# Kernel optimization log

Measured on AMD Instinct MI355X. Metric: run time of the kernel, lower is better.

## Reference

```python
import jax, jax.numpy as jnp
import numpy as np
import itertools

B, G, FEAT, IMG = 2048, 8, 512, 1024
SCALES = list(range(G, 1, -1))  # [8,7,6,5,4,3,2]
SUBSAMPLE = 12


def setup_inputs() -> dict:
    key = jax.random.key(0)
    keys = jax.random.split(key, 1 + 2 * len(SCALES))
    rng = np.random.default_rng(0)
    inp = {"input": jax.random.normal(keys[0], (B, G, FEAT), dtype=jnp.float32)}
    for i, scale in enumerate(SCALES):
        perms = np.array(list(itertools.permutations(range(G), scale)), dtype=np.int32)
        n_sub = min(SUBSAMPLE, len(perms))
        sel = rng.choice(len(perms), n_sub, replace=False)
        inp[f"perms{i}"] = jnp.asarray(perms[sel])  # [n_sub, scale] int32
        lim = 1.0 / np.sqrt(scale * FEAT)
        inp[f"W{i}"] = jax.random.uniform(keys[1 + 2 * i], (IMG, scale * FEAT), minval=-lim, maxval=lim, dtype=jnp.float32)
        inp[f"b{i}"] = jax.random.uniform(keys[2 + 2 * i], (IMG,), minval=-lim, maxval=lim, dtype=jnp.float32)
    return inp


def _forward(input, perms_list, W_list, b_list):
    outs = []
    for perms, W, b in zip(perms_list, W_list, b_list):
        # gather: [B, n_sub, scale, FEAT] -> [B, n_sub, scale*FEAT]
        g = input[:, perms, :]
        g = g.reshape(g.shape[0], g.shape[1], -1)
        # batched linear over all subsamples, then mean over subsamples
        y = jnp.einsum('bsf,df->bsd', g, W) + b  # [B, n_sub, IMG]
        outs.append(y.mean(axis=1))
    return jnp.concatenate(outs, axis=1)  # [B, len(SCALES)*IMG]


def reference(input, perms0, W0, b0, perms1, W1, b1, perms2, W2, b2,
              perms3, W3, b3, perms4, W4, b4, perms5, W5, b5, perms6, W6, b6):
    perms_list = [perms0, perms1, perms2, perms3, perms4, perms5, perms6]
    W_list = [W0, W1, W2, W3, W4, W5, W6]
    b_list = [b0, b1, b2, b3, b4, b5, b6]
    return _forward(input, perms_list, W_list, b_list)
```

## Files before the change

### kernel.cpp

```cpp
#include <hip/hip_runtime.h>

typedef unsigned short u16;
typedef __bf16 bf16x8 __attribute__((ext_vector_type(8)));
typedef float f32x4 __attribute__((ext_vector_type(4)));

__device__ __forceinline__ u16 f2bf(float f) {
  unsigned int u = __float_as_uint(f);
  return (u16)((u + 0x7fffu + ((u >> 16) & 1u)) >> 16);
}


__global__ __launch_bounds__(256) void k_prep(
    const float* __restrict__ x,
    const int* p0, const int* p1, const int* p2, const int* p3,
    const int* p4, const int* p5, const int* p6,
    const float* W0, const float* W1, const float* W2, const float* W3,
    const float* W4, const float* W5, const float* W6,
    u16* __restrict__ Xb16, u16* __restrict__ Wtil) {
  __shared__ float sC[64];
  const int bid = blockIdx.x;
  const int t = threadIdx.x;
  if (bid < 1792) {
    const int r0 = bid << 2;
    const int i = r0 >> 10;
    const int scale = 8 - i;
    const int K = scale << 9;
    const int d0 = r0 - (i << 10);
    if (t < 64) {
      const int g = t >> 3, j = t & 7;
      float v = 0.f;
      if (j < scale) {
        const int* p = (i == 0) ? p0 : (i == 1) ? p1 : (i == 2) ? p2 :
                       (i == 3) ? p3 : (i == 4) ? p4 : (i == 5) ? p5 : p6;
        int cnt = 0;
        for (int s = 0; s < 12; ++s) cnt += (p[s * scale + j] == g) ? 1 : 0;
        v = (float)cnt * (1.0f / 12.0f);
      }
      sC[t] = v;
    }
    __syncthreads();
    const float* Wi = (i == 0) ? W0 : (i == 1) ? W1 : (i == 2) ? W2 :
                      (i == 3) ? W3 : (i == 4) ? W4 : (i == 5) ? W5 : W6;
    const int u = t & 63;
    const int gq = t >> 6;
    u16* dst = Wtil + ((size_t)r0 << 12);
    for (int r = 0; r < 4; ++r) {
      const float* wrow = Wi + (size_t)(d0 + r) * K;
      float a0[8], a1[8];
#pragma unroll
      for (int e = 0; e < 8; ++e) { a0[e] = 0.f; a1[e] = 0.f; }
      for (int j = 0; j < scale; ++j) {
        const float* wp = wrow + j * 512 + (u << 3);
        const float4 wa = *reinterpret_cast<const float4*>(wp);
        const float4 wb = *reinterpret_cast<const float4*>(wp + 4);
        const float c0 = sC[(gq << 4) + j];
        const float c1 = sC[(gq << 4) + 8 + j];
        a0[0] += c0 * wa.x; a0[1] += c0 * wa.y; a0[2] += c0 * wa.z; a0[3] += c0 * wa.w;
        a0[4] += c0 * wb.x; a0[5] += c0 * wb.y; a0[6] += c0 * wb.z; a0[7] += c0 * wb.w;
        a1[0] += c1 * wa.x; a1[1] += c1 * wa.y; a1[2] += c1 * wa.z; a1[3] += c1 * wa.w;
        a1[4] += c1 * wb.x; a1[5] += c1 * wb.y; a1[6] += c1 * wb.z; a1[7] += c1 * wb.w;
      }
      uint4 o0, o1;
      o0.x = (unsigned)f2bf(a0[0]) | ((unsigned)f2bf(a0[1]) << 16);
      o0.y = (unsigned)f2bf(a0[2]) | ((unsigned)f2bf(a0[3]) << 16);
      o0.z = (unsigned)f2bf(a0[4]) | ((unsigned)f2bf(a0[5]) << 16);
      o0.w = (unsigned)f2bf(a0[6]) | ((unsigned)f2bf(a0[7]) << 16);
      o1.x = (unsigned)f2bf(a1[0]) | ((unsigned)f2bf(a1[1]) << 16);
      o1.y = (unsigned)f2bf(a1[2]) | ((unsigned)f2bf(a1[3]) << 16);
      o1.z = (unsigned)f2bf(a1[4]) | ((unsigned)f2bf(a1[5]) << 16);
      o1.w = (unsigned)f2bf(a1[6]) | ((unsigned)f2bf(a1[7]) << 16);
      u16* drow = dst + ((size_t)r << 12) + (gq << 10) + (u << 3);
      *reinterpret_cast<uint4*>(drow) = o0;
      *reinterpret_cast<uint4*>(drow + 512) = o1;
    }
  } else {
    const int tid0 = ((bid - 1792) << 8) | t;
    const float4* X4 = reinterpret_cast<const float4*>(x);
    uint4* O = reinterpret_cast<uint4*>(Xb16);
#pragma unroll 4
    for (int it = 0; it < 16; ++it) {
      const int e = tid0 + (it << 16);
      const float4 a = X4[(size_t)e * 2];
      const float4 c = X4[(size_t)e * 2 + 1];
      uint4 o;
      o.x = (unsigned)f2bf(a.x) | ((unsigned)f2bf(a.y) << 16);
      o.y = (unsigned)f2bf(a.z) | ((unsigned)f2bf(a.w) << 16);
      o.z = (unsigned)f2bf(c.x) | ((unsigned)f2bf(c.y) << 16);
      o.w = (unsigned)f2bf(c.z) | ((unsigned)f2bf(c.w) << 16);
      O[e] = o;
    }
  }
}

__device__ __forceinline__ void gl_lds16(const u16* g, u16* l) {
  __builtin_amdgcn_global_load_lds(
      (const __attribute__((address_space(1))) void*)g,
      (__attribute__((address_space(3))) void*)l, 16, 0, 0);
}

#define WAIT_VM10  0x0F7A
#define WAIT_VM8   0x0F78
#define WAIT_VM4   0x0F74
#define WAIT_VM2   0x0F72
#define WAIT_VM0   0x0F70
#define WAIT_LGKM0 0xC07F

#define MFMA_Q(QD, AV, BV)                                                   \
  _Pragma("unroll")                                                          \
  for (int mf_ = 0; mf_ < 4; ++mf_) {                                        \
    _Pragma("unroll")                                                        \
    for (int nf_ = 0; nf_ < 2; ++nf_) {                                      \
      acc[QD][mf_][nf_] = __builtin_amdgcn_mfma_f32_16x16x32_bf16(           \
          AV[mf_][0], BV[nf_][0], acc[QD][mf_][nf_], 0, 0, 0);               \
      acc[QD][mf_][nf_] = __builtin_amdgcn_mfma_f32_16x16x32_bf16(           \
          AV[mf_][1], BV[nf_][1], acc[QD][mf_][nf_], 0, 0, 0);               \
    }                                                                        \
  }

#define RD_A(BASE)                                                           \
  _Pragma("unroll")                                                          \
  for (int mf_ = 0; mf_ < 4; ++mf_) {                                        \
    aR[mf_][0] = *reinterpret_cast<const bf16x8*>(lds + (BASE) + offA[mf_]);        \
    aR[mf_][1] = *reinterpret_cast<const bf16x8*>(lds + (BASE) + (offA[mf_] ^ 32)); \
  }

#define RD_B(BASE, ARR)                                                      \
  _Pragma("unroll")                                                          \
  for (int nf_ = 0; nf_ < 2; ++nf_) {                                        \
    ARR[nf_][0] = *reinterpret_cast<const bf16x8*>(lds + (BASE) + offB[nf_]);        \
    ARR[nf_][1] = *reinterpret_cast<const bf16x8*>(lds + (BASE) + (offB[nf_] ^ 32)); \
  }

#define PH_BAR  __builtin_amdgcn_s_barrier()
#define PH_LGKM __builtin_amdgcn_s_waitcnt(WAIT_LGKM0)
#define PRIO1   __builtin_amdgcn_s_setprio(1)
#define PRIO0   __builtin_amdgcn_s_setprio(0)

__global__ __launch_bounds__(512, 2) void k_gemm(
    const u16* __restrict__ A, const u16* __restrict__ Bm,
    const float* b0, const float* b1, const float* b2, const float* b3,
    const float* b4, const float* b5, const float* b6,
    float* __restrict__ out) {
  __shared__ u16 lds[65536];
  const int bid = blockIdx.x;
  const int blockM = (bid & 7) * 256;
  const int blockN = (bid >> 3) * 256;

  const int tid = threadIdx.x;
  const int lane = tid & 63;
  const int wid = tid >> 6;
  const int wm = (wid >> 2) * 64;
  const int wn = (wid & 3) * 32;
  const int quad = lane >> 4;
  const int l15 = lane & 15;

  const int srow = tid >> 3;
  const int sslot = tid & 7;
  const int gch = (sslot - srow) & 7;
  const u16* gA0 = A + (size_t)(blockM + srow) * 4096 + gch * 8;
  const u16* gB0 = Bm + (size_t)(blockN + srow) * 4096 + gch * 8;

  int offA[4], offB[2];
#pragma unroll
  for (int mf = 0; mf < 4; ++mf) {
    const int r = wm + mf * 16 + l15;
    offA[mf] = r * 64 + ((quad + r) & 7) * 8;
  }
#pragma unroll
  for (int nf = 0; nf < 2; ++nf) {
    const int r = wn + nf * 16 + l15;
    offB[nf] = 16384 + r * 64 + ((quad + r) & 7) * 8;
  }

  f32x4 acc[4][4][2];
#pragma unroll
  for (int q = 0; q < 4; ++q)
#pragma unroll
    for (int m = 0; m < 4; ++m)
#pragma unroll
      for (int n = 0; n < 2; ++n) {
        f32x4 z = {0.f, 0.f, 0.f, 0.f};
        acc[q][m][n] = z;
      }

  auto stage = [&](int mat, int h, int t, int db) {
    const u16* g = (mat ? gB0 : gA0) + (size_t)h * (128 * 4096) + (size_t)t * 64;
    u16* l = lds + db + mat * 16384 + h * 8192 + (tid << 3);
    gl_lds16(g, l);
    gl_lds16(g + (size_t)(64 * 4096), l + 4096);
  };

  stage(0, 0, 0, 0); stage(1, 0, 0, 0); stage(1, 1, 0, 0); stage(0, 1, 0, 0);
  stage(0, 0, 1, 32768); stage(1, 0, 1, 32768); stage(1, 1, 1, 32768);
  __builtin_amdgcn_s_waitcnt(WAIT_VM10);
  PH_BAR;

  bf16x8 aR[4][2], bL[2][2], bH[2][2];

  for (int j = 0; j < 31; ++j) {
    const int t1 = 2 * j + 1;
    const int t2 = 2 * j + 2;
    const int t3 = 2 * j + 3;

    RD_A(0) RD_B(0, bL)
    stage(0, 1, t1, 32768);
    PH_BAR; PH_LGKM; PRIO1; MFMA_Q(0, aR, bL) PRIO0;
    __builtin_amdgcn_s_waitcnt(WAIT_VM10); PH_BAR;

    RD_B(8192, bH)
    stage(0, 0, t2, 0);
    PH_BAR; PH_LGKM; PRIO1; MFMA_Q(1, aR, bH) PRIO0;
    __builtin_amdgcn_s_waitcnt(WAIT_VM10); PH_BAR;

    RD_A(8192)
    stage(1, 0, t2, 0);
    PH_BAR; PH_LGKM; PRIO1; MFMA_Q(2, aR, bH) PRIO0;
    PH_BAR;

    stage(1, 1, t2, 0);
    PH_BAR; PRIO1; MFMA_Q(3, aR, bL) PRIO0;
    __builtin_amdgcn_s_waitcnt(WAIT_VM10); PH_BAR;

    RD_A(32768) RD_B(32768, bL)
    stage(0, 1, t2, 0);
    PH_BAR; PH_LGKM; PRIO1; MFMA_Q(0, aR, bL) PRIO0;
    __builtin_amdgcn_s_waitcnt(WAIT_VM10); PH_BAR;

    RD_B(32768 + 8192, bH)
    stage(0, 0, t3, 32768);
    PH_BAR; PH_LGKM; PRIO1; MFMA_Q(1, aR, bH) PRIO0;
    __builtin_amdgcn_s_waitcnt(WAIT_VM10); PH_BAR;

    RD_A(32768 + 8192)
    stage(1, 0, t3, 32768);
    PH_BAR; PH_LGKM; PRIO1; MFMA_Q(2, aR, bH) PRIO0;
    PH_BAR;

    stage(1, 1, t3, 32768);
    PH_BAR; PRIO1; MFMA_Q(3, aR, bL) PRIO0;
    __builtin_amdgcn_s_waitcnt(WAIT_VM10); PH_BAR;
  }

  {
    RD_A(0) RD_B(0, bL)
    stage(0, 1, 63, 32768);
    PH_BAR; PH_LGKM; PRIO1; MFMA_Q(0, aR, bL) PRIO0;
    __builtin_amdgcn_s_waitcnt(WAIT_VM10); PH_BAR;

    RD_B(8192, bH)
    PH_BAR; PH_LGKM; PRIO1; MFMA_Q(1, aR, bH) PRIO0;
    __builtin_amdgcn_s_waitcnt(WAIT_VM8); PH_BAR;

    RD_A(8192)
    PH_BAR; PH_LGKM; PRIO1; MFMA_Q(2, aR, bH) PRIO0;
    PH_BAR;

    PH_BAR; PRIO1; MFMA_Q(3, aR, bL) PRIO0;
    __builtin_amdgcn_s_waitcnt(WAIT_VM4); PH_BAR;

    RD_A(32768) RD_B(32768, bL)
    PH_BAR; PH_LGKM; PRIO1; MFMA_Q(0, aR, bL) PRIO0;
    __builtin_amdgcn_s_waitcnt(WAIT_VM2); PH_BAR;

    RD_B(32768 + 8192, bH)
    PH_BAR; PH_LGKM; PRIO1; MFMA_Q(1, aR, bH) PRIO0;
    __builtin_amdgcn_s_waitcnt(WAIT_VM0); PH_BAR;

    RD_A(32768 + 8192)
    PH_BAR; PH_LGKM; PRIO1; MFMA_Q(2, aR, bH) PRIO0;
    PH_BAR;

    PRIO1; MFMA_Q(3, aR, bL) PRIO0;
  }

  const int isc = blockN >> 10;
  const float* bi = (isc == 0) ? b0 : (isc == 1) ? b1 : (isc == 2) ? b2 :
                    (isc == 3) ? b3 : (isc == 4) ? b4 : (isc == 5) ? b5 : b6;
#pragma unroll
  for (int qd = 0; qd < 4; ++qd) {
    const int Mq = (qd >= 2) ? 128 : 0;
    const int Nq = (qd == 1 || qd == 2) ? 128 : 0;
#pragma unroll
    for (int nf = 0; nf < 2; ++nf) {
      const int ncol = blockN + Nq + wn + nf * 16 + l15;
      const float bias = bi[ncol & 1023];
#pragma unroll
      for (int mf = 0; mf < 4; ++mf) {
        const int mbase = blockM + Mq + wm + mf * 16 + quad * 4;
#pragma unroll
        for (int reg = 0; reg < 4; ++reg)
          out[(size_t)(mbase + reg) * 7168 + ncol] = acc[qd][mf][nf][reg] + bias;
      }
    }
  }
}

extern "C" void kernel_launch(void* const* d_in, const int* in_sizes, int n_in,
                              void* d_out, int out_size, void* d_ws, size_t ws_size,
                              hipStream_t stream) {
  const float* input = (const float*)d_in[0];
  const int* perms[7];
  const float* W[7];
  const float* bias[7];
  for (int i = 0; i < 7; ++i) {
    perms[i] = (const int*)d_in[1 + 3 * i];
    W[i]     = (const float*)d_in[2 + 3 * i];
    bias[i]  = (const float*)d_in[3 + 3 * i];
  }
  char* ws = (char*)d_ws;
  u16* Xb16 = (u16*)ws;
  u16* Wtil = (u16*)(ws + (size_t)2048 * 4096 * 2);

  k_prep<<<2048, 256, 0, stream>>>(input,
                                   perms[0], perms[1], perms[2], perms[3],
                                   perms[4], perms[5], perms[6],
                                   W[0], W[1], W[2], W[3], W[4], W[5], W[6],
                                   Xb16, Wtil);
  k_gemm<<<224, 512, 0, stream>>>(Xb16, Wtil,
                                  bias[0], bias[1], bias[2], bias[3],
                                  bias[4], bias[5], bias[6],
                                  (float*)d_out);
}
```

Baseline: 298.2 us.

## Switch GEMM to 32x32x16 MFMA with register double-buffered LDS fragment prefetch

Replaces the 16x16x32 bf16 MFMA tiles with 32x32x16 MFMAs, so each wave computes 64x32 sub-tiles with fewer, larger instructions and fewer LDS fragment reads per FLOP. The LDS offsets and swizzle are recomputed for the new fragment layout, and the epilogue is rewritten to match the 32x32 accumulator row mapping. The phase schedule is restructured to prefetch A/B fragments into separate lo/hi register sets one phase ahead, removing explicit LGKM waits and some barriers, and the vmcnt thresholds change. This lowers LDS traffic and issue overhead but increases register pressure and makes correctness depend on the retimed waits and barriers.

```diff
diff --git a/kernel.cpp b/kernel.cpp
--- a/kernel.cpp
+++ b/kernel.cpp
@@ -2,7 +2,7 @@
 
 typedef unsigned short u16;
 typedef __bf16 bf16x8 __attribute__((ext_vector_type(8)));
-typedef float f32x4 __attribute__((ext_vector_type(4)));
+typedef float f32x16 __attribute__((ext_vector_type(16)));
 
 __device__ __forceinline__ u16 f2bf(float f) {
   unsigned int u = __float_as_uint(f);
@@ -98,43 +98,35 @@
       (__attribute__((address_space(3))) void*)l, 16, 0, 0);
 }
 
-#define WAIT_VM10  0x0F7A
-#define WAIT_VM8   0x0F78
-#define WAIT_VM4   0x0F74
-#define WAIT_VM2   0x0F72
-#define WAIT_VM0   0x0F70
-#define WAIT_LGKM0 0xC07F
-
-#define MFMA_Q(QD, AV, BV)                                                   \
+#define VM6 __builtin_amdgcn_s_waitcnt(0x0F76)
+#define VM4 __builtin_amdgcn_s_waitcnt(0x0F74)
+#define VM2 __builtin_amdgcn_s_waitcnt(0x0F72)
+#define VM0 __builtin_amdgcn_s_waitcnt(0x0F70)
+#define BAR __builtin_amdgcn_s_barrier()
+#define PRIO1 __builtin_amdgcn_s_setprio(1)
+#define PRIO0 __builtin_amdgcn_s_setprio(0)
+
+#define RD_A_(dst, BASE)                                                     \
   _Pragma("unroll")                                                          \
-  for (int mf_ = 0; mf_ < 4; ++mf_) {                                        \
+  for (int mf_ = 0; mf_ < 2; ++mf_)                                          \
     _Pragma("unroll")                                                        \
-    for (int nf_ = 0; nf_ < 2; ++nf_) {                                      \
-      acc[QD][mf_][nf_] = __builtin_amdgcn_mfma_f32_16x16x32_bf16(           \
-          AV[mf_][0], BV[nf_][0], acc[QD][mf_][nf_], 0, 0, 0);               \
-      acc[QD][mf_][nf_] = __builtin_amdgcn_mfma_f32_16x16x32_bf16(           \
-          AV[mf_][1], BV[nf_][1], acc[QD][mf_][nf_], 0, 0, 0);               \
-    }                                                                        \
-  }
-
-#define RD_A(BASE)                                                           \
+    for (int kk_ = 0; kk_ < 4; ++kk_)                                        \
+      dst[mf_][kk_] = *reinterpret_cast<const bf16x8*>(lds + (BASE) + offA[mf_][kk_]);
+
+#define RD_B_(dst, BASE)                                                     \
   _Pragma("unroll")                                                          \
-  for (int mf_ = 0; mf_ < 4; ++mf_) {                                        \
-    aR[mf_][0] = *reinterpret_cast<const bf16x8*>(lds + (BASE) + offA[mf_]);        \
-    aR[mf_][1] = *reinterpret_cast<const bf16x8*>(lds + (BASE) + (offA[mf_] ^ 32)); \
-  }
-
-#define RD_B(BASE, ARR)                                                      \
+  for (int kk_ = 0; kk_ < 4; ++kk_)                                          \
+    dst[kk_] = *reinterpret_cast<const bf16x8*>(lds + (BASE) + offB[kk_]);
+
+#define MFMA_Q(QD, AH, BH)                                                   \
+  PRIO1;                                                                     \
   _Pragma("unroll")                                                          \
-  for (int nf_ = 0; nf_ < 2; ++nf_) {                                        \
-    ARR[nf_][0] = *reinterpret_cast<const bf16x8*>(lds + (BASE) + offB[nf_]);        \
-    ARR[nf_][1] = *reinterpret_cast<const bf16x8*>(lds + (BASE) + (offB[nf_] ^ 32)); \
-  }
-
-#define PH_BAR  __builtin_amdgcn_s_barrier()
-#define PH_LGKM __builtin_amdgcn_s_waitcnt(WAIT_LGKM0)
-#define PRIO1   __builtin_amdgcn_s_setprio(1)
-#define PRIO0   __builtin_amdgcn_s_setprio(0)
+  for (int mf_ = 0; mf_ < 2; ++mf_)                                          \
+    _Pragma("unroll")                                                        \
+    for (int kk_ = 0; kk_ < 4; ++kk_)                                        \
+      acc[QD][mf_] = __builtin_amdgcn_mfma_f32_32x32x16_bf16(                \
+          AH[mf_][kk_], BH[kk_], acc[QD][mf_], 0, 0, 0);                     \
+  PRIO0;
 
 __global__ __launch_bounds__(512, 2) void k_gemm(
     const u16* __restrict__ A, const u16* __restrict__ Bm,
@@ -151,8 +143,8 @@
   const int wid = tid >> 6;
   const int wm = (wid >> 2) * 64;
   const int wn = (wid & 3) * 32;
-  const int quad = lane >> 4;
-  const int l15 = lane & 15;
+  const int l31 = lane & 31;
+  const int hi = lane >> 5;
 
   const int srow = tid >> 3;
   const int sslot = tid & 7;
@@ -160,28 +152,27 @@
   const u16* gA0 = A + (size_t)(blockM + srow) * 4096 + gch * 8;
   const u16* gB0 = Bm + (size_t)(blockN + srow) * 4096 + gch * 8;
 
-  int offA[4], offB[2];
-#pragma unroll
-  for (int mf = 0; mf < 4; ++mf) {
-    const int r = wm + mf * 16 + l15;
-    offA[mf] = r * 64 + ((quad + r) & 7) * 8;
-  }
-#pragma unroll
-  for (int nf = 0; nf < 2; ++nf) {
-    const int r = wn + nf * 16 + l15;
-    offB[nf] = 16384 + r * 64 + ((quad + r) & 7) * 8;
-  }
-
-  f32x4 acc[4][4][2];
+  int offA[2][4], offB[4];
+#pragma unroll
+  for (int mf = 0; mf < 2; ++mf)
+#pragma unroll
+    for (int kk = 0; kk < 4; ++kk) {
+      const int r = wm + mf * 32 + l31;
+      offA[mf][kk] = r * 64 + (((2 * kk + hi) + r) & 7) * 8;
+    }
+#pragma unroll
+  for (int kk = 0; kk < 4; ++kk) {
+    const int r = wn + l31;
+    offB[kk] = r * 64 + (((2 * kk + hi) + r) & 7) * 8;
+  }
+
+  f32x16 acc[4][2];
 #pragma unroll
   for (int q = 0; q < 4; ++q)
 #pragma unroll
-    for (int m = 0; m < 4; ++m)
-#pragma unroll
-      for (int n = 0; n < 2; ++n) {
-        f32x4 z = {0.f, 0.f, 0.f, 0.f};
-        acc[q][m][n] = z;
-      }
+    for (int m = 0; m < 2; ++m)
+#pragma unroll
+      for (int e = 0; e < 16; ++e) acc[q][m][e] = 0.f;
 
   auto stage = [&](int mat, int h, int t, int db) {
     const u16* g = (mat ? gB0 : gA0) + (size_t)h * (128 * 4096) + (size_t)t * 64;
@@ -190,87 +181,92 @@
     gl_lds16(g + (size_t)(64 * 4096), l + 4096);
   };
 
+  bf16x8 aLo[2][4], aHi[2][4], bLo[4], bHi[4];
+
   stage(0, 0, 0, 0); stage(1, 0, 0, 0); stage(1, 1, 0, 0); stage(0, 1, 0, 0);
-  stage(0, 0, 1, 32768); stage(1, 0, 1, 32768); stage(1, 1, 1, 32768);
-  __builtin_amdgcn_s_waitcnt(WAIT_VM10);
-  PH_BAR;
-
-  bf16x8 aR[4][2], bL[2][2], bH[2][2];
+  stage(0, 0, 1, 32768); stage(1, 1, 1, 32768);
+  VM0;
+  BAR;
+  RD_A_(aLo, 0)
+  RD_B_(bLo, 16384)
 
   for (int j = 0; j < 31; ++j) {
     const int t1 = 2 * j + 1;
     const int t2 = 2 * j + 2;
     const int t3 = 2 * j + 3;
 
-    RD_A(0) RD_B(0, bL)
+    RD_B_(bHi, 24576)
+    stage(1, 0, t1, 32768);
+    MFMA_Q(0, aLo, bLo)
+    VM6; BAR;
+
+    RD_A_(aHi, 8192)
     stage(0, 1, t1, 32768);
-    PH_BAR; PH_LGKM; PRIO1; MFMA_Q(0, aR, bL) PRIO0;
-    __builtin_amdgcn_s_waitcnt(WAIT_VM10); PH_BAR;
-
-    RD_B(8192, bH)
+    MFMA_Q(1, aLo, bHi)
+    VM6; BAR;
+
+    RD_A_(aLo, 32768)
     stage(0, 0, t2, 0);
-    PH_BAR; PH_LGKM; PRIO1; MFMA_Q(1, aR, bH) PRIO0;
-    __builtin_amdgcn_s_waitcnt(WAIT_VM10); PH_BAR;
-
-    RD_A(8192)
+    MFMA_Q(2, aHi, bHi)
+    VM4; BAR;
+
+    stage(1, 1, t2, 0);
+    MFMA_Q(3, aHi, bLo)
+    RD_B_(bLo, 32768 + 16384)
+    BAR;
+
+    RD_B_(bHi, 32768 + 24576)
     stage(1, 0, t2, 0);
-    PH_BAR; PH_LGKM; PRIO1; MFMA_Q(2, aR, bH) PRIO0;
-    PH_BAR;
-
-    stage(1, 1, t2, 0);
-    PH_BAR; PRIO1; MFMA_Q(3, aR, bL) PRIO0;
-    __builtin_amdgcn_s_waitcnt(WAIT_VM10); PH_BAR;
-
-    RD_A(32768) RD_B(32768, bL)
+    MFMA_Q(0, aLo, bLo)
+    VM6; BAR;
+
+    RD_A_(aHi, 32768 + 8192)
     stage(0, 1, t2, 0);
-    PH_BAR; PH_LGKM; PRIO1; MFMA_Q(0, aR, bL) PRIO0;
-    __builtin_amdgcn_s_waitcnt(WAIT_VM10); PH_BAR;
-
-    RD_B(32768 + 8192, bH)
+    MFMA_Q(1, aLo, bHi)
+    VM6; BAR;
+
+    RD_A_(aLo, 0)
     stage(0, 0, t3, 32768);
-    PH_BAR; PH_LGKM; PRIO1; MFMA_Q(1, aR, bH) PRIO0;
-    __builtin_amdgcn_s_waitcnt(WAIT_VM10); PH_BAR;
-
-    RD_A(32768 + 8192)
-    stage(1, 0, t3, 32768);
-    PH_BAR; PH_LGKM; PRIO1; MFMA_Q(2, aR, bH) PRIO0;
-    PH_BAR;
+    MFMA_Q(2, aHi, bHi)
+    VM4; BAR;
 
     stage(1, 1, t3, 32768);
-    PH_BAR; PRIO1; MFMA_Q(3, aR, bL) PRIO0;
-    __builtin_amdgcn_s_waitcnt(WAIT_VM10); PH_BAR;
+    MFMA_Q(3, aHi, bLo)
+    RD_B_(bLo, 16384)
+    BAR;
   }
 
   {
-    RD_A(0) RD_B(0, bL)
+    RD_B_(bHi, 24576)
+    stage(1, 0, 63, 32768);
+    MFMA_Q(0, aLo, bLo)
+    VM6; BAR;
+
+    RD_A_(aHi, 8192)
     stage(0, 1, 63, 32768);
-    PH_BAR; PH_LGKM; PRIO1; MFMA_Q(0, aR, bL) PRIO0;
-    __builtin_amdgcn_s_waitcnt(WAIT_VM10); PH_BAR;
-
-    RD_B(8192, bH)
-    PH_BAR; PH_LGKM; PRIO1; MFMA_Q(1, aR, bH) PRIO0;
-    __builtin_amdgcn_s_waitcnt(WAIT_VM8); PH_BAR;
-
-    RD_A(8192)
-    PH_BAR; PH_LGKM; PRIO1; MFMA_Q(2, aR, bH) PRIO0;
-    PH_BAR;
-
-    PH_BAR; PRIO1; MFMA_Q(3, aR, bL) PRIO0;
-    __builtin_amdgcn_s_waitcnt(WAIT_VM4); PH_BAR;
-
-    RD_A(32768) RD_B(32768, bL)
-    PH_BAR; PH_LGKM; PRIO1; MFMA_Q(0, aR, bL) PRIO0;
-    __builtin_amdgcn_s_waitcnt(WAIT_VM2); PH_BAR;
-
-    RD_B(32768 + 8192, bH)
-    PH_BAR; PH_LGKM; PRIO1; MFMA_Q(1, aR, bH) PRIO0;
-    __builtin_amdgcn_s_waitcnt(WAIT_VM0); PH_BAR;
-
-    RD_A(32768 + 8192)
-    PH_BAR; PH_LGKM; PRIO1; MFMA_Q(2, aR, bH) PRIO0;
-    PH_BAR;
-
-    PRIO1; MFMA_Q(3, aR, bL) PRIO0;
+    MFMA_Q(1, aLo, bHi)
+    VM6; BAR;
+
+    RD_A_(aLo, 32768)
+    MFMA_Q(2, aHi, bHi)
+    VM2; BAR;
+
+    MFMA_Q(3, aHi, bLo)
+    RD_B_(bLo, 32768 + 16384)
+    BAR;
+
+    RD_B_(bHi, 32768 + 24576)
+    MFMA_Q(0, aLo, bLo)
+    VM0; BAR;
+
+    RD_A_(aHi, 32768 + 8192)
+    MFMA_Q(1, aLo, bHi)
+    BAR;
+
+    MFMA_Q(2, aHi, bHi)
+    BAR;
+
+    MFMA_Q(3, aHi, bLo)
   }
 
   const int isc = blockN >> 10;
@@ -280,16 +276,15 @@
   for (int qd = 0; qd < 4; ++qd) {
     const int Mq = (qd >= 2) ? 128 : 0;
     const int Nq = (qd == 1 || qd == 2) ? 128 : 0;
-#pragma unroll
-    for (int nf = 0; nf < 2; ++nf) {
-      const int ncol = blockN + Nq + wn + nf * 16 + l15;
-      const float bias = bi[ncol & 1023];
-#pragma unroll
-      for (int mf = 0; mf < 4; ++mf) {
-        const int mbase = blockM + Mq + wm + mf * 16 + quad * 4;
-#pragma unroll
-        for (int reg = 0; reg < 4; ++reg)
-          out[(size_t)(mbase + reg) * 7168 + ncol] = acc[qd][mf][nf][reg] + bias;
+    const int col = blockN + Nq + wn + l31;
+    const float bias = bi[col & 1023];
+#pragma unroll
+    for (int mf = 0; mf < 2; ++mf) {
+      const int rbase = blockM + Mq + wm + mf * 32 + 4 * hi;
+#pragma unroll
+      for (int reg = 0; reg < 16; ++reg) {
+        const int row = rbase + (reg & 3) + 8 * (reg >> 2);
+        out[(size_t)row * 7168 + col] = acc[qd][mf][reg] + bias;
       }
     }
   }
```

New measurement: 314.0 us. 5.3% more time.
